# Optimization experiments

Hardware: AMD Instinct MI355X
Metric: run time of the kernel (lower is better)

Reference implementation:

```python
import jax, jax.numpy as jnp
import numpy as np

B, H, W, L, C = 4, 64, 64, 64, 64
NB, BS, F = 8, 8, 1          # num_blocks, block_size, hidden_size_factor
R, ALPHA = 8, 1.0            # lora_r, lora_alpha
M, T = 32, 8                 # modes, temporal_modes
SCALE = 1.0 / (BS * BS * F)  # param init scale from the module


def setup_inputs() -> dict:
    key = jax.random.key(0)
    ks = jax.random.split(key, 14)
    d = {"x": jax.random.normal(ks[0], (B, H, W, L, C), jnp.float32)}
    d["w1"] = SCALE * jax.random.uniform(ks[1], (2, NB, BS, BS * F), jnp.float32)
    d["b1"] = SCALE * jax.random.uniform(ks[2], (2, NB, BS * F), jnp.float32)
    d["w2"] = SCALE * jax.random.uniform(ks[3], (2, NB, BS * F, BS), jnp.float32)
    d["b2"] = SCALE * jax.random.uniform(ks[4], (2, NB, BS), jnp.float32)
    names = ["la1rA", "la1rB", "la1iA", "la1iB", "la2rA", "la2rB", "la2iA", "la2iB"]
    shapes = [(NB, BS, R), (NB, R, BS * F), (NB, BS, R), (NB, R, BS * F),
              (NB, BS * F, R), (NB, R, BS), (NB, BS * F, R), (NB, R, BS)]
    for i, (n, s) in enumerate(zip(names, shapes)):
        d[n] = 0.02 * jax.random.normal(ks[5 + i], s, jnp.float32)
    return d


def _afno(x, w1, b1, w2, b2, la1rA, la1rB, la1iA, la1iB, la2rA, la2rB, la2iA, la2iB):
    s = ALPHA / R
    # effective per-block weights: base + LoRA low-rank update  [NB, in, out]
    W1r = w1[0] + s * jnp.einsum('nir,nro->nio', la1rA, la1rB)
    W1i = w1[1] + s * jnp.einsum('nir,nro->nio', la1iA, la1iB)
    W2r = w2[0] + s * jnp.einsum('nir,nro->nio', la2rA, la2rB)
    W2i = w2[1] + s * jnp.einsum('nir,nro->nio', la2iA, la2iB)

    xf = jnp.fft.rfftn(x, axes=(1, 2, 3), norm='ortho')      # [B,H,W,L//2+1,C] complex
    Lh = xf.shape[3]
    xs = xf[:, :M, :M, :T].reshape(B, M, M, T, NB, BS)        # truncated modes, block split
    xr, xi = xs.real, xs.imag

    def lin(v, Wb, bb):  # block-diagonal linear: [...,n,i] x [n,i,o] + [n,o]
        return jnp.einsum('bxyzni,nio->bxyzno', v, Wb) + bb

    gelu = lambda t: jax.nn.gelu(t, approximate=False)
    o1r = gelu(lin(xr, W1r, b1[0]) - lin(xi, W1i, b1[1]))
    o1i = gelu(lin(xi, W1r, b1[0]) + lin(xr, W1i, b1[1]))
    o2r = lin(o1r, W2r, b2[0]) - lin(o1i, W2i, b2[1])
    o2i = lin(o1i, W2r, b2[0]) + lin(o1r, W2i, b2[1])

    o2 = (o2r + 1j * o2i).reshape(B, M, M, T, C)
    full = jnp.zeros((B, H, W, Lh, C), dtype=xf.dtype).at[:, :M, :M, :T].set(o2)
    out = jnp.fft.irfftn(full, s=(H, W, L), axes=(1, 2, 3), norm='ortho')
    return out + x


def reference(x, w1, b1, w2, b2, la1rA, la1rB, la1iA, la1iB, la2rA, la2rB, la2iA, la2iB):
    return _afno(x, w1, b1, w2, b2, la1rA, la1rB, la1iA, la1iB, la2rA, la2rB, la2iA, la2iB)
```

## Files before the change

### kernel.cpp

```cpp
#include <hip/hip_runtime.h>
#include <math.h>


#define PI2_64 0.09817477042468103f

__device__ __forceinline__ float gelu_exact(float t) {
    return 0.5f * t * (1.0f + erff(t * 0.7071067811865475f));
}

__device__ __forceinline__ unsigned int f2bf(float f) {
    unsigned int u = __float_as_uint(f);
    return (u + 0x7FFFu + ((u >> 16) & 1u)) >> 16;
}
__device__ __forceinline__ uint2 pack4(float4 f) {
    return make_uint2(f2bf(f.x) | (f2bf(f.y) << 16),
                      f2bf(f.z) | (f2bf(f.w) << 16));
}
__device__ __forceinline__ float4 unpack4(uint2 u) {
    return make_float4(__uint_as_float(u.x << 16),
                       __uint_as_float(u.x & 0xFFFF0000u),
                       __uint_as_float(u.y << 16),
                       __uint_as_float(u.y & 0xFFFF0000u));
}

__global__ void __launch_bounds__(256) k1a_dft_l(const float* __restrict__ x,
                                                 unsigned int* __restrict__ y1f) {
    __shared__ float2 twT[8][32];
    int tid = threadIdx.x;
    if (tid < 256) {
        int k = tid >> 5, l = tid & 31;
        float s, c;
        sincosf(PI2_64 * (float)((k * l) & 63), &s, &c);
        twT[k][l] = make_float2(c, s);
    }
    __syncthreads();

    int bid = blockIdx.x;
    int wg = bid & 3, bh = bid >> 2;
    int cq = tid & 15, wl = tid >> 4;
    int w = wg * 16 + wl;
    const float* xp = x + (size_t)(bh * 64 + w) * 4096 + 4 * cq;

    float4 A0[8], A1[8];
#pragma unroll
    for (int kl = 0; kl < 8; ++kl) {
        A0[kl] = make_float4(0.f, 0.f, 0.f, 0.f);
        A1[kl] = make_float4(0.f, 0.f, 0.f, 0.f);
    }

    for (int l0 = 0; l0 < 32; l0 += 2) {
        float4 v0  = *(const float4*)(xp + (l0 + 0) * 64);
        float4 v0p = *(const float4*)(xp + (l0 + 32) * 64);
        float4 v1  = *(const float4*)(xp + (l0 + 1) * 64);
        float4 v1p = *(const float4*)(xp + (l0 + 33) * 64);
        float4 E0 = make_float4(v0.x + v0p.x, v0.y + v0p.y, v0.z + v0p.z, v0.w + v0p.w);
        float4 O0 = make_float4(v0.x - v0p.x, v0.y - v0p.y, v0.z - v0p.z, v0.w - v0p.w);
        float4 E1 = make_float4(v1.x + v1p.x, v1.y + v1p.y, v1.z + v1p.z, v1.w + v1p.w);
        float4 O1 = make_float4(v1.x - v1p.x, v1.y - v1p.y, v1.z - v1p.z, v1.w - v1p.w);
#pragma unroll
        for (int kl = 0; kl < 8; ++kl) {
            float2 t0 = twT[kl][l0];
            float2 t1 = twT[kl][l0 + 1];
            float4 s0 = (kl & 1) ? O0 : E0;
            float4 s1 = (kl & 1) ? O1 : E1;
            A0[kl].x += s0.x * t0.x;  A0[kl].y -= s0.x * t0.y;
            A0[kl].z += s0.y * t0.x;  A0[kl].w -= s0.y * t0.y;
            A1[kl].x += s0.z * t0.x;  A1[kl].y -= s0.z * t0.y;
            A1[kl].z += s0.w * t0.x;  A1[kl].w -= s0.w * t0.y;
            A0[kl].x += s1.x * t1.x;  A0[kl].y -= s1.x * t1.y;
            A0[kl].z += s1.y * t1.x;  A0[kl].w -= s1.y * t1.y;
            A1[kl].x += s1.z * t1.x;  A1[kl].y -= s1.z * t1.y;
            A1[kl].z += s1.w * t1.x;  A1[kl].w -= s1.w * t1.y;
        }
    }
    uint4* y1 = (uint4*)y1f;
    size_t base = (size_t)bh * 8192 + (size_t)w * 16 + cq;
#pragma unroll
    for (int kl = 0; kl < 8; ++kl) {
        uint2 p0 = pack4(A0[kl]);
        uint2 p1 = pack4(A1[kl]);
        y1[base + kl * 1024] = make_uint4(p0.x, p0.y, p1.x, p1.y);
    }
}

__global__ void __launch_bounds__(256) k1b_dft_w(const unsigned int* __restrict__ y1f,
                                                 unsigned int* __restrict__ y2f) {
    __shared__ float4 sD[64 * 32];
    __shared__ float2 twT[32][32];
    int tid = threadIdx.x;
#pragma unroll
    for (int e = 0; e < 4; ++e) {
        int idx = e * 256 + tid;
        int k = idx >> 5, l = idx & 31;
        float s, c;
        sincosf(PI2_64 * (float)((k * l) & 63), &s, &c);
        twT[k][l] = make_float2(c, s);
    }
    int pos = blockIdx.x;
    int kl = pos & 7, bh = pos >> 3;
    const uint2* src = (const uint2*)y1f + (size_t)pos * 2048;
#pragma unroll
    for (int r = 0; r < 8; ++r)
        sD[r * 256 + tid] = unpack4(src[r * 256 + tid]);
    __syncthreads();

    int cp = tid & 31, kwg = tid >> 5;
    float4 acc[4];
#pragma unroll
    for (int i = 0; i < 4; ++i) acc[i] = make_float4(0.f, 0.f, 0.f, 0.f);

    for (int w = 0; w < 32; ++w) {
        float4 d  = sD[w * 32 + cp];
        float4 dp = sD[(w + 32) * 32 + cp];
        float4 E = make_float4(d.x + dp.x, d.y + dp.y, d.z + dp.z, d.w + dp.w);
        float4 O = make_float4(d.x - dp.x, d.y - dp.y, d.z - dp.z, d.w - dp.w);
#pragma unroll
        for (int i = 0; i < 4; ++i) {
            float2 t = twT[kwg * 4 + i][w];
            float4 s = (i & 1) ? O : E;
            acc[i].x += s.x * t.x + s.y * t.y;
            acc[i].y += s.y * t.x - s.x * t.y;
            acc[i].z += s.z * t.x + s.w * t.y;
            acc[i].w += s.w * t.x - s.z * t.y;
        }
    }
    int b = bh >> 6, h = bh & 63;
    uint2* y2 = (uint2*)y2f;
#pragma unroll
    for (int i = 0; i < 4; ++i) {
        int kw = kwg * 4 + i;
        y2[((size_t)((b * 8 + kl) * 32 + kw) * 64 + h) * 32 + cp] = pack4(acc[i]);
    }
}

__global__ void __launch_bounds__(256) kc_h_mlp(
        const unsigned int* __restrict__ y2f, unsigned int* __restrict__ z2f,
        const float* __restrict__ w1, const float* __restrict__ b1,
        const float* __restrict__ w2, const float* __restrict__ b2,
        const float* __restrict__ la1rA, const float* __restrict__ la1rB,
        const float* __restrict__ la1iA, const float* __restrict__ la1iB,
        const float* __restrict__ la2rA, const float* __restrict__ la2rB,
        const float* __restrict__ la2iA, const float* __restrict__ la2iB) {
    __shared__ float2 sD[64][64];
    __shared__ float2 sT[32][34];
    __shared__ float2 sM[32][66];
    __shared__ float  sW[4][512];
    __shared__ float  sb1[128], sb2[128];
    int tid = threadIdx.x;
    int pos = blockIdx.x;
    int kl = pos & 7, kw = (pos >> 3) & 31, b = pos >> 8;

#pragma unroll
    for (int r = 0; r < 4; ++r) {
        int idx = r * 256 + tid;
        int h = idx >> 5, kh = idx & 31;
        float sn, cs;
        sincosf(PI2_64 * (float)((h * kh) & 63), &sn, &cs);
        sT[h][kh] = make_float2(cs, -sn);
    }
    const uint2* src = (const uint2*)y2f + (size_t)((b * 8 + kl) * 32 + kw) * 2048;
#pragma unroll
    for (int r = 0; r < 8; ++r) {
        int idx = r * 256 + tid;
        *(float4*)(&sD[idx >> 5][(idx & 31) * 2]) = unpack4(src[idx]);
    }
    {
        const float* As[4]   = {la1rA, la1iA, la2rA, la2iA};
        const float* Bs[4]   = {la1rB, la1iB, la2rB, la2iB};
        const float* base[4] = {w1, w1 + 512, w2, w2 + 512};
#pragma unroll
        for (int e = 0; e < 8; ++e) {
            int flat = tid + e * 256;
            int mat = flat >> 9;
            int rem = flat & 511;
            int n = rem >> 6, i = (rem >> 3) & 7, o = rem & 7;
            const float* A  = As[mat] + n * 64 + i * 8;
            const float* Bp = Bs[mat] + n * 64 + o;
            float s = 0.f;
#pragma unroll
            for (int r = 0; r < 8; ++r) s += A[r] * Bp[r * 8];
            sW[mat][(i * 8 + o) * 8 + n] = base[mat][n * 64 + i * 8 + o] + 0.125f * s;
        }
        if (tid < 128) sb1[tid] = b1[tid];
        else           sb2[tid - 128] = b2[tid - 128];
    }
    __syncthreads();

    {
        float4* sd4 = (float4*)&sD[0][0];
#pragma unroll
        for (int r = 0; r < 4; ++r) {
            int idx = r * 256 + tid;
            int h = idx >> 5, cq = idx & 31;
            float4 a = sd4[h * 32 + cq];
            float4 c = sd4[(h + 32) * 32 + cq];
            sd4[h * 32 + cq]        = make_float4(a.x + c.x, a.y + c.y, a.z + c.z, a.w + c.w);
            sd4[(h + 32) * 32 + cq] = make_float4(a.x - c.x, a.y - c.y, a.z - c.z, a.w - c.w);
        }
    }
    __syncthreads();

    {
        int kh0 = (tid >> 5) * 4;
        int c0  = (tid & 31) * 2;
        float mr[4][2], mi[4][2];
#pragma unroll
        for (int i = 0; i < 4; ++i)
#pragma unroll
            for (int j = 0; j < 2; ++j) { mr[i][j] = 0.f; mi[i][j] = 0.f; }
        for (int h = 0; h < 32; ++h) {
            float4 dE = *(const float4*)(&sD[h][c0]);
            float4 dO = *(const float4*)(&sD[h + 32][c0]);
            float Er[2] = {dE.x, dE.z}, Ei[2] = {dE.y, dE.w};
            float Or[2] = {dO.x, dO.z}, Oi[2] = {dO.y, dO.w};
            const float4* tT = (const float4*)(&sT[h][kh0]);
            float4 u0 = tT[0], u1 = tT[1];
            float Tr[4] = {u0.x, u0.z, u1.x, u1.z};
            float Ti[4] = {u0.y, u0.w, u1.y, u1.w};
#pragma unroll
            for (int i = 0; i < 4; ++i) {
                const float* Dr = (i & 1) ? Or : Er;
                const float* Di = (i & 1) ? Oi : Ei;
#pragma unroll
                for (int j = 0; j < 2; ++j) {
                    mr[i][j] += Tr[i] * Dr[j] - Ti[i] * Di[j];
                    mi[i][j] += Tr[i] * Di[j] + Ti[i] * Dr[j];
                }
            }
        }
        const float sc = 1.0f / 512.0f;
#pragma unroll
        for (int i = 0; i < 4; ++i)
#pragma unroll
            for (int j = 0; j < 2; ++j)
                sM[kh0 + i][c0 + j] = make_float2(mr[i][j] * sc, mi[i][j] * sc);
    }
    __syncthreads();

    float2* sM2 = (float2*)&sD[0][0];
    {
        int kh = tid >> 3, n = tid & 7;
        float xr[8], xi[8];
#pragma unroll
        for (int i = 0; i < 8; ++i) {
            float2 v = sM[kh][n * 8 + i];
            xr[i] = v.x; xi[i] = v.y;
        }
        float o1r[8], o1i[8];
#pragma unroll
        for (int o = 0; o < 8; ++o) {
            float br = sb1[n * 8 + o], bi = sb1[64 + n * 8 + o];
            float sr = br - bi, si = br + bi;
#pragma unroll
            for (int i = 0; i < 8; ++i) {
                float wr = sW[0][(i * 8 + o) * 8 + n];
                float wi = sW[1][(i * 8 + o) * 8 + n];
                sr += xr[i] * wr - xi[i] * wi;
                si += xi[i] * wr + xr[i] * wi;
            }
            o1r[o] = gelu_exact(sr);
            o1i[o] = gelu_exact(si);
        }
#pragma unroll
        for (int o = 0; o < 8; ++o) {
            float br = sb2[n * 8 + o], bi = sb2[64 + n * 8 + o];
            float sr = br - bi, si = br + bi;
#pragma unroll
            for (int i = 0; i < 8; ++i) {
                float wr = sW[2][(i * 8 + o) * 8 + n];
                float wi = sW[3][(i * 8 + o) * 8 + n];
                sr += o1r[i] * wr - o1i[i] * wi;
                si += o1i[i] * wr + o1r[i] * wi;
            }
            sM2[kh * 66 + n * 8 + o] = make_float2(sr, si);
        }
    }
    __syncthreads();

    {
        int h0 = (tid >> 4) * 2;
        int c0 = (tid & 15) * 4;
        float SEr[2][4], SEi[2][4], SOr[2][4], SOi[2][4];
#pragma unroll
        for (int r = 0; r < 2; ++r)
#pragma unroll
            for (int j = 0; j < 4; ++j) {
                SEr[r][j] = 0.f; SEi[r][j] = 0.f;
                SOr[r][j] = 0.f; SOi[r][j] = 0.f;
            }
        for (int khp = 0; khp < 16; ++khp) {
#pragma unroll
            for (int par = 0; par < 2; ++par) {
                int kh = 2 * khp + par;
                float2 T0 = sT[h0 + 0][kh];
                float2 T1 = sT[h0 + 1][kh];
                const float4* tM = (const float4*)(sM2 + kh * 66 + c0);
                float4 m0 = tM[0], m1 = tM[1];
                float Mr[4] = {m0.x, m0.z, m1.x, m1.z};
                float Mi[4] = {m0.y, m0.w, m1.y, m1.w};
                float (*Sr)[4] = par ? SOr : SEr;
                float (*Si)[4] = par ? SOi : SEi;
                float Tr[2] = {T0.x, T1.x};
                float Ti[2] = {T0.y, T1.y};
#pragma unroll
                for (int r = 0; r < 2; ++r)
#pragma unroll
                    for (int j = 0; j < 4; ++j) {
                        Sr[r][j] += Tr[r] * Mr[j] + Ti[r] * Mi[j];
                        Si[r][j] += Tr[r] * Mi[j] - Ti[r] * Mr[j];
                    }
            }
        }
        uint2* dst = (uint2*)z2f + (size_t)((b * 8 + kl) * 32 + kw) * 2048;
#pragma unroll
        for (int r = 0; r < 2; ++r) {
            int iA = (h0 + r) * 32 + (c0 >> 1);
            dst[iA]     = pack4(make_float4(SEr[r][0] + SOr[r][0], SEi[r][0] + SOi[r][0],
                                            SEr[r][1] + SOr[r][1], SEi[r][1] + SOi[r][1]));
            dst[iA + 1] = pack4(make_float4(SEr[r][2] + SOr[r][2], SEi[r][2] + SOi[r][2],
                                            SEr[r][3] + SOr[r][3], SEi[r][3] + SOi[r][3]));
            int iB = (h0 + 32 + r) * 32 + (c0 >> 1);
            dst[iB]     = pack4(make_float4(SEr[r][0] - SOr[r][0], SEi[r][0] - SOi[r][0],
                                            SEr[r][1] - SOr[r][1], SEi[r][1] - SOi[r][1]));
            dst[iB + 1] = pack4(make_float4(SEr[r][2] - SOr[r][2], SEi[r][2] - SOi[r][2],
                                            SEr[r][3] - SOr[r][3], SEi[r][3] - SOi[r][3]));
        }
    }
}

__global__ void __launch_bounds__(256) k3a_idft_w(const unsigned int* __restrict__ z2f,
                                                  unsigned int* __restrict__ zwf) {
    __shared__ float4 sZ[2 * 32 * 32];
    __shared__ float2 twT[32][32];
    int tid = threadIdx.x;
#pragma unroll
    for (int e = 0; e < 4; ++e) {
        int idx = e * 256 + tid;
        int w = idx >> 5, kw = idx & 31;
        float s, c;
        sincosf(PI2_64 * (float)((w * kw) & 63), &s, &c);
        twT[w][kw] = make_float2(c, s);
    }
    int bid = blockIdx.x;
    int klq = bid & 3, h = (bid >> 2) & 63, b = bid >> 8;
    const uint2* z2 = (const uint2*)z2f;
#pragma unroll
    for (int r = 0; r < 8; ++r) {
        int idx = r * 256 + tid;
        int row = idx >> 5, cp2 = idx & 31;
        int kli = row >> 5, kw = row & 31;
        sZ[idx] = unpack4(
            z2[((size_t)((b * 8 + klq * 2 + kli) * 32 + kw) * 64 + h) * 32 + cp2]);
    }
    __syncthreads();

    int cp = tid & 31, wq = tid >> 5;

    float4 E[2][4], O[2][4];
#pragma unroll
    for (int kli = 0; kli < 2; ++kli)
#pragma unroll
        for (int j = 0; j < 4; ++j) {
            E[kli][j] = make_float4(0.f, 0.f, 0.f, 0.f);
            O[kli][j] = make_float4(0.f, 0.f, 0.f, 0.f);
        }

    for (int kw = 0; kw < 32; kw += 2) {
#pragma unroll
        for (int kli = 0; kli < 2; ++kli) {
            float4 d = sZ[(kli * 32 + kw) * 32 + cp];
#pragma unroll
            for (int j = 0; j < 4; ++j) {
                float2 t = twT[wq * 4 + j][kw];
                E[kli][j].x += d.x * t.x - d.y * t.y;
                E[kli][j].y += d.y * t.x + d.x * t.y;
                E[kli][j].z += d.z * t.x - d.w * t.y;
                E[kli][j].w += d.w * t.x + d.z * t.y;
            }
        }
#pragma unroll
        for (int kli = 0; kli < 2; ++kli) {
            float4 d = sZ[(kli * 32 + kw + 1) * 32 + cp];
#pragma unroll
            for (int j = 0; j < 4; ++j) {
                float2 t = twT[wq * 4 + j][kw + 1];
                O[kli][j].x += d.x * t.x - d.y * t.y;
                O[kli][j].y += d.y * t.x + d.x * t.y;
                O[kli][j].z += d.z * t.x - d.w * t.y;
                O[kli][j].w += d.w * t.x + d.z * t.y;
            }
        }
    }
    uint2* zw = (uint2*)zwf;
    size_t slab = ((size_t)(b * 64 + h)) * 16384;
#pragma unroll
    for (int kli = 0; kli < 2; ++kli) {
        int kl = klq * 2 + kli;
#pragma unroll
        for (int j = 0; j < 4; ++j) {
            int w = wq * 4 + j;
            float4 e = E[kli][j], o = O[kli][j];
            zw[slab + ((size_t)w * 8 + kl) * 32 + cp] =
                pack4(make_float4(e.x + o.x, e.y + o.y, e.z + o.z, e.w + o.w));
            zw[slab + ((size_t)(w + 32) * 8 + kl) * 32 + cp] =
                pack4(make_float4(e.x - o.x, e.y - o.y, e.z - o.z, e.w - o.w));
        }
    }
}

__global__ void __launch_bounds__(256) k3b_idft_l(const float* __restrict__ x,
                                                  const unsigned int* __restrict__ zwf,
                                                  float* __restrict__ outp) {
    __shared__ float2 twA[8][32];
    int tid = threadIdx.x;
    if (tid < 256) {
        int k = tid >> 5, l = tid & 31;
        float s, c;
        sincosf(PI2_64 * (float)((k * l) & 63), &s, &c);
        twA[k][l] = make_float2(c, s);
    }
    __syncthreads();

    int bid = blockIdx.x;
    int wg = bid & 3, bh = bid >> 2;
    int cq = tid & 15, wl = tid >> 4;
    int w = wg * 16 + wl;

    const uint4* zw4 = (const uint4*)zwf;
    size_t zbase = ((size_t)(bh * 64 + w)) * 128 + cq;
    float4 z0[8], z1[8];
#pragma unroll
    for (int kl = 0; kl < 8; ++kl) {
        uint4 u = zw4[zbase + kl * 16];
        z0[kl] = unpack4(make_uint2(u.x, u.y));
        z1[kl] = unpack4(make_uint2(u.z, u.w));
    }

    float r00 = z0[0].x, r01 = z0[0].z;
    float r10 = z1[0].x, r11 = z1[0].z;
#pragma unroll
    for (int kl = 1; kl < 8; ++kl) {
        z0[kl].x *= 2.f; z0[kl].y *= 2.f; z0[kl].z *= 2.f; z0[kl].w *= 2.f;
        z1[kl].x *= 2.f; z1[kl].y *= 2.f; z1[kl].z *= 2.f; z1[kl].w *= 2.f;
    }
    const size_t row = ((size_t)(bh * 64 + w)) * 4096;
    const float* xp = x + row + 4 * cq;
    float* op = outp + row + 4 * cq;
    const float sc = 1.0f / 512.0f;

    for (int l = 0; l < 32; ++l) {
        float4 a0 = *(const float4*)(xp + l * 64);
        float4 a1 = *(const float4*)(xp + (l + 32) * 64);
        float e00 = 0.f, e01 = 0.f, e10 = 0.f, e11 = 0.f;
        float o00 = 0.f, o01 = 0.f, o10 = 0.f, o11 = 0.f;
#pragma unroll
        for (int kl = 2; kl < 8; kl += 2) {
            float2 t = twA[kl][l];
            e00 += z0[kl].x * t.x - z0[kl].y * t.y;
            e01 += z0[kl].z * t.x - z0[kl].w * t.y;
            e10 += z1[kl].x * t.x - z1[kl].y * t.y;
            e11 += z1[kl].z * t.x - z1[kl].w * t.y;
        }
#pragma unroll
        for (int kl = 1; kl < 8; kl += 2) {
            float2 t = twA[kl][l];
            o00 += z0[kl].x * t.x - z0[kl].y * t.y;
            o01 += z0[kl].z * t.x - z0[kl].w * t.y;
            o10 += z1[kl].x * t.x - z1[kl].y * t.y;
            o11 += z1[kl].z * t.x - z1[kl].w * t.y;
        }
        float b00 = r00 + e00, b01 = r01 + e01;
        float b10 = r10 + e10, b11 = r11 + e11;
        *(float4*)(op + l * 64) = make_float4(
            (b00 + o00) * sc + a0.x, (b01 + o01) * sc + a0.y,
            (b10 + o10) * sc + a0.z, (b11 + o11) * sc + a0.w);
        *(float4*)(op + (l + 32) * 64) = make_float4(
            (b00 - o00) * sc + a1.x, (b01 - o01) * sc + a1.y,
            (b10 - o10) * sc + a1.z, (b11 - o11) * sc + a1.w);
    }
}

extern "C" void kernel_launch(void* const* d_in, const int* in_sizes, int n_in,
                              void* d_out, int out_size, void* d_ws, size_t ws_size,
                              hipStream_t stream) {
    const float* x     = (const float*)d_in[0];
    const float* w1    = (const float*)d_in[1];
    const float* b1    = (const float*)d_in[2];
    const float* w2    = (const float*)d_in[3];
    const float* b2    = (const float*)d_in[4];
    const float* la1rA = (const float*)d_in[5];
    const float* la1rB = (const float*)d_in[6];
    const float* la1iA = (const float*)d_in[7];
    const float* la1iB = (const float*)d_in[8];
    const float* la2rA = (const float*)d_in[9];
    const float* la2rB = (const float*)d_in[10];
    const float* la2iA = (const float*)d_in[11];
    const float* la2iB = (const float*)d_in[12];
    float* out = (float*)d_out;

    unsigned int* ws = (unsigned int*)d_ws;
    unsigned int* y1 = ws;
    unsigned int* y2 = ws + 8388608;
    unsigned int* z2 = ws + 12582912;
    unsigned int* zw = ws + 16777216;

    hipLaunchKernelGGL(k1a_dft_l,  dim3(1024), dim3(256), 0, stream, x, y1);
    hipLaunchKernelGGL(k1b_dft_w,  dim3(2048), dim3(256), 0, stream, y1, y2);
    hipLaunchKernelGGL(kc_h_mlp,   dim3(1024), dim3(256), 0, stream, y2, z2,
                       w1, b1, w2, b2, la1rA, la1rB, la1iA, la1iB,
                       la2rA, la2rB, la2iA, la2iB);
    hipLaunchKernelGGL(k3a_idft_w, dim3(1024), dim3(256), 0, stream, z2, zw);
    hipLaunchKernelGGL(k3b_idft_l, dim3(1024), dim3(256), 0, stream, x, zw, out);
}
```

Before: 306.1 us.

## Fuse L and W forward DFT kernels via shared memory, keep mlp buffers bf16

```diff
diff --git a/kernel.cpp b/kernel.cpp
--- a/kernel.cpp
+++ b/kernel.cpp
@@ -22,114 +22,106 @@
                        __uint_as_float(u.y << 16),
                        __uint_as_float(u.y & 0xFFFF0000u));
 }
-
-__global__ void __launch_bounds__(256) k1a_dft_l(const float* __restrict__ x,
-                                                 unsigned int* __restrict__ y1f) {
-    __shared__ float2 twT[8][32];
+__device__ __forceinline__ unsigned int pack2(float r, float i) {
+    return f2bf(r) | (f2bf(i) << 16);
+}
+__device__ __forceinline__ float2 unpack2(unsigned int u) {
+    return make_float2(__uint_as_float(u << 16),
+                       __uint_as_float(u & 0xFFFF0000u));
+}
+
+__global__ void __launch_bounds__(256) k1_fused(const float* __restrict__ x,
+                                                unsigned int* __restrict__ y2f) {
+    __shared__ uint2  sY[8 * 1089];
+    __shared__ float2 twT1[8][32];
+    __shared__ float2 twT2[32][32];
     int tid = threadIdx.x;
-    if (tid < 256) {
+    {
         int k = tid >> 5, l = tid & 31;
         float s, c;
         sincosf(PI2_64 * (float)((k * l) & 63), &s, &c);
-        twT[k][l] = make_float2(c, s);
-    }
-    __syncthreads();
-
-    int bid = blockIdx.x;
-    int wg = bid & 3, bh = bid >> 2;
-    int cq = tid & 15, wl = tid >> 4;
-    int w = wg * 16 + wl;
-    const float* xp = x + (size_t)(bh * 64 + w) * 4096 + 4 * cq;
-
-    float4 A0[8], A1[8];
-#pragma unroll
-    for (int kl = 0; kl < 8; ++kl) {
-        A0[kl] = make_float4(0.f, 0.f, 0.f, 0.f);
-        A1[kl] = make_float4(0.f, 0.f, 0.f, 0.f);
-    }
-
-    for (int l0 = 0; l0 < 32; l0 += 2) {
-        float4 v0  = *(const float4*)(xp + (l0 + 0) * 64);
-        float4 v0p = *(const float4*)(xp + (l0 + 32) * 64);
-        float4 v1  = *(const float4*)(xp + (l0 + 1) * 64);
-        float4 v1p = *(const float4*)(xp + (l0 + 33) * 64);
-        float4 E0 = make_float4(v0.x + v0p.x, v0.y + v0p.y, v0.z + v0p.z, v0.w + v0p.w);
-        float4 O0 = make_float4(v0.x - v0p.x, v0.y - v0p.y, v0.z - v0p.z, v0.w - v0p.w);
-        float4 E1 = make_float4(v1.x + v1p.x, v1.y + v1p.y, v1.z + v1p.z, v1.w + v1p.w);
-        float4 O1 = make_float4(v1.x - v1p.x, v1.y - v1p.y, v1.z - v1p.z, v1.w - v1p.w);
-#pragma unroll
-        for (int kl = 0; kl < 8; ++kl) {
-            float2 t0 = twT[kl][l0];
-            float2 t1 = twT[kl][l0 + 1];
-            float4 s0 = (kl & 1) ? O0 : E0;
-            float4 s1 = (kl & 1) ? O1 : E1;
-            A0[kl].x += s0.x * t0.x;  A0[kl].y -= s0.x * t0.y;
-            A0[kl].z += s0.y * t0.x;  A0[kl].w -= s0.y * t0.y;
-            A1[kl].x += s0.z * t0.x;  A1[kl].y -= s0.z * t0.y;
-            A1[kl].z += s0.w * t0.x;  A1[kl].w -= s0.w * t0.y;
-            A0[kl].x += s1.x * t1.x;  A0[kl].y -= s1.x * t1.y;
-            A0[kl].z += s1.y * t1.x;  A0[kl].w -= s1.y * t1.y;
-            A1[kl].x += s1.z * t1.x;  A1[kl].y -= s1.z * t1.y;
-            A1[kl].z += s1.w * t1.x;  A1[kl].w -= s1.w * t1.y;
-        }
-    }
-    uint4* y1 = (uint4*)y1f;
-    size_t base = (size_t)bh * 8192 + (size_t)w * 16 + cq;
-#pragma unroll
-    for (int kl = 0; kl < 8; ++kl) {
-        uint2 p0 = pack4(A0[kl]);
-        uint2 p1 = pack4(A1[kl]);
-        y1[base + kl * 1024] = make_uint4(p0.x, p0.y, p1.x, p1.y);
-    }
-}
-
-__global__ void __launch_bounds__(256) k1b_dft_w(const unsigned int* __restrict__ y1f,
-                                                 unsigned int* __restrict__ y2f) {
-    __shared__ float4 sD[64 * 32];
-    __shared__ float2 twT[32][32];
-    int tid = threadIdx.x;
+        twT1[k][l] = make_float2(c, s);
+    }
 #pragma unroll
     for (int e = 0; e < 4; ++e) {
         int idx = e * 256 + tid;
         int k = idx >> 5, l = idx & 31;
         float s, c;
         sincosf(PI2_64 * (float)((k * l) & 63), &s, &c);
-        twT[k][l] = make_float2(c, s);
-    }
-    int pos = blockIdx.x;
-    int kl = pos & 7, bh = pos >> 3;
-    const uint2* src = (const uint2*)y1f + (size_t)pos * 2048;
-#pragma unroll
-    for (int r = 0; r < 8; ++r)
-        sD[r * 256 + tid] = unpack4(src[r * 256 + tid]);
-    __syncthreads();
-
-    int cp = tid & 31, kwg = tid >> 5;
-    float4 acc[4];
-#pragma unroll
-    for (int i = 0; i < 4; ++i) acc[i] = make_float4(0.f, 0.f, 0.f, 0.f);
-
-    for (int w = 0; w < 32; ++w) {
-        float4 d  = sD[w * 32 + cp];
-        float4 dp = sD[(w + 32) * 32 + cp];
-        float4 E = make_float4(d.x + dp.x, d.y + dp.y, d.z + dp.z, d.w + dp.w);
-        float4 O = make_float4(d.x - dp.x, d.y - dp.y, d.z - dp.z, d.w - dp.w);
-#pragma unroll
-        for (int i = 0; i < 4; ++i) {
-            float2 t = twT[kwg * 4 + i][w];
-            float4 s = (i & 1) ? O : E;
-            acc[i].x += s.x * t.x + s.y * t.y;
-            acc[i].y += s.y * t.x - s.x * t.y;
-            acc[i].z += s.z * t.x + s.w * t.y;
-            acc[i].w += s.w * t.x - s.z * t.y;
-        }
-    }
-    int b = bh >> 6, h = bh & 63;
-    uint2* y2 = (uint2*)y2f;
-#pragma unroll
-    for (int i = 0; i < 4; ++i) {
-        int kw = kwg * 4 + i;
-        y2[((size_t)((b * 8 + kl) * 32 + kw) * 64 + h) * 32 + cp] = pack4(acc[i]);
+        twT2[k][l] = make_float2(c, s);
+    }
+    __syncthreads();
+
+    int bid = blockIdx.x;
+    int ch = bid & 1, bh = bid >> 1;
+
+    {
+        int cp = tid & 15, wl = tid >> 4;
+#pragma unroll
+        for (int wi = 0; wi < 4; ++wi) {
+            int w = wi * 16 + wl;
+            const float* xp = x + (size_t)(bh * 64 + w) * 4096 + ch * 32 + 2 * cp;
+            float4 A[8];
+#pragma unroll
+            for (int kl = 0; kl < 8; ++kl) A[kl] = make_float4(0.f, 0.f, 0.f, 0.f);
+            for (int l0 = 0; l0 < 32; l0 += 2) {
+                float2 v0  = *(const float2*)(xp + (l0 + 0) * 64);
+                float2 v0p = *(const float2*)(xp + (l0 + 32) * 64);
+                float2 v1  = *(const float2*)(xp + (l0 + 1) * 64);
+                float2 v1p = *(const float2*)(xp + (l0 + 33) * 64);
+                float2 E0 = make_float2(v0.x + v0p.x, v0.y + v0p.y);
+                float2 O0 = make_float2(v0.x - v0p.x, v0.y - v0p.y);
+                float2 E1 = make_float2(v1.x + v1p.x, v1.y + v1p.y);
+                float2 O1 = make_float2(v1.x - v1p.x, v1.y - v1p.y);
+#pragma unroll
+                for (int kl = 0; kl < 8; ++kl) {
+                    float2 t0 = twT1[kl][l0];
+                    float2 t1 = twT1[kl][l0 + 1];
+                    float2 s0 = (kl & 1) ? O0 : E0;
+                    float2 s1 = (kl & 1) ? O1 : E1;
+                    A[kl].x += s0.x * t0.x;  A[kl].y -= s0.x * t0.y;
+                    A[kl].z += s0.y * t0.x;  A[kl].w -= s0.y * t0.y;
+                    A[kl].x += s1.x * t1.x;  A[kl].y -= s1.x * t1.y;
+                    A[kl].z += s1.y * t1.x;  A[kl].w -= s1.y * t1.y;
+                }
+            }
+#pragma unroll
+            for (int kl = 0; kl < 8; ++kl)
+                sY[kl * 1089 + w * 17 + cp] = pack4(A[kl]);
+        }
+    }
+    __syncthreads();
+
+    {
+        int cp = tid & 15, kl = (tid >> 4) & 7, kwh = tid >> 7;
+        const uint2* row = &sY[kl * 1089];
+        float4 acc[16];
+#pragma unroll
+        for (int i = 0; i < 16; ++i) acc[i] = make_float4(0.f, 0.f, 0.f, 0.f);
+
+        for (int w = 0; w < 32; ++w) {
+            float4 a = unpack4(row[w * 17 + cp]);
+            float4 b4 = unpack4(row[(w + 32) * 17 + cp]);
+            float4 E = make_float4(a.x + b4.x, a.y + b4.y, a.z + b4.z, a.w + b4.w);
+            float4 O = make_float4(a.x - b4.x, a.y - b4.y, a.z - b4.z, a.w - b4.w);
+#pragma unroll
+            for (int i = 0; i < 16; ++i) {
+                float2 t = twT2[kwh * 16 + i][w];
+                float4 s = (i & 1) ? O : E;
+                acc[i].x += s.x * t.x + s.y * t.y;
+                acc[i].y += s.y * t.x - s.x * t.y;
+                acc[i].z += s.z * t.x + s.w * t.y;
+                acc[i].w += s.w * t.x - s.z * t.y;
+            }
+        }
+        int b = bh >> 6, h = bh & 63;
+        uint2* y2 = (uint2*)y2f;
+#pragma unroll
+        for (int i = 0; i < 16; ++i) {
+            int kw = kwh * 16 + i;
+            y2[((size_t)((b * 8 + kl) * 32 + kw) * 64 + h) * 32 + ch * 16 + cp] =
+                pack4(acc[i]);
+        }
     }
 }
 
@@ -141,11 +133,12 @@
         const float* __restrict__ la1iA, const float* __restrict__ la1iB,
         const float* __restrict__ la2rA, const float* __restrict__ la2rB,
         const float* __restrict__ la2iA, const float* __restrict__ la2iB) {
-    __shared__ float2 sD[64][64];
+    __shared__ uint2  sDu[64 * 32];
     __shared__ float2 sT[32][34];
-    __shared__ float2 sM[32][66];
+    __shared__ unsigned int sMu[32 * 66];
     __shared__ float  sW[4][512];
     __shared__ float  sb1[128], sb2[128];
+    unsigned int* sM2u = (unsigned int*)sDu;
     int tid = threadIdx.x;
     int pos = blockIdx.x;
     int kl = pos & 7, kw = (pos >> 3) & 31, b = pos >> 8;
@@ -162,7 +155,7 @@
 #pragma unroll
     for (int r = 0; r < 8; ++r) {
         int idx = r * 256 + tid;
-        *(float4*)(&sD[idx >> 5][(idx & 31) * 2]) = unpack4(src[idx]);
+        sDu[idx] = src[idx];
     }
     {
         const float* As[4]   = {la1rA, la1iA, la2rA, la2iA};
@@ -187,32 +180,21 @@
     __syncthreads();
 
     {
-        float4* sd4 = (float4*)&sD[0][0];
-#pragma unroll
-        for (int r = 0; r < 4; ++r) {
-            int idx = r * 256 + tid;
-            int h = idx >> 5, cq = idx & 31;
-            float4 a = sd4[h * 32 + cq];
-            float4 c = sd4[(h + 32) * 32 + cq];
-            sd4[h * 32 + cq]        = make_float4(a.x + c.x, a.y + c.y, a.z + c.z, a.w + c.w);
-            sd4[(h + 32) * 32 + cq] = make_float4(a.x - c.x, a.y - c.y, a.z - c.z, a.w - c.w);
-        }
-    }
-    __syncthreads();
-
-    {
         int kh0 = (tid >> 5) * 4;
-        int c0  = (tid & 31) * 2;
+        int cq  = tid & 31;
+        int c0f = cq * 2;
         float mr[4][2], mi[4][2];
 #pragma unroll
         for (int i = 0; i < 4; ++i)
 #pragma unroll
             for (int j = 0; j < 2; ++j) { mr[i][j] = 0.f; mi[i][j] = 0.f; }
         for (int h = 0; h < 32; ++h) {
-            float4 dE = *(const float4*)(&sD[h][c0]);
-            float4 dO = *(const float4*)(&sD[h + 32][c0]);
-            float Er[2] = {dE.x, dE.z}, Ei[2] = {dE.y, dE.w};
-            float Or[2] = {dO.x, dO.z}, Oi[2] = {dO.y, dO.w};
+            float4 a  = unpack4(sDu[h * 32 + cq]);
+            float4 c4 = unpack4(sDu[(h + 32) * 32 + cq]);
+            float Er[2] = {a.x + c4.x, a.z + c4.z};
+            float Ei[2] = {a.y + c4.y, a.w + c4.w};
+            float Or[2] = {a.x - c4.x, a.z - c4.z};
+            float Oi[2] = {a.y - c4.y, a.w - c4.w};
             const float4* tT = (const float4*)(&sT[h][kh0]);
             float4 u0 = tT[0], u1 = tT[1];
             float Tr[4] = {u0.x, u0.z, u1.x, u1.z};
@@ -233,17 +215,16 @@
         for (int i = 0; i < 4; ++i)
 #pragma unroll
             for (int j = 0; j < 2; ++j)
-                sM[kh0 + i][c0 + j] = make_float2(mr[i][j] * sc, mi[i][j] * sc);
-    }
-    __syncthreads();
-
-    float2* sM2 = (float2*)&sD[0][0];
+                sMu[(kh0 + i) * 66 + c0f + j] = pack2(mr[i][j] * sc, mi[i][j] * sc);
+    }
+    __syncthreads();
+
     {
         int kh = tid >> 3, n = tid & 7;
         float xr[8], xi[8];
 #pragma unroll
         for (int i = 0; i < 8; ++i) {
-            float2 v = sM[kh][n * 8 + i];
+            float2 v = unpack2(sMu[kh * 66 + n * 8 + i]);
             xr[i] = v.x; xi[i] = v.y;
         }
         float o1r[8], o1i[8];
@@ -272,7 +253,7 @@
                 sr += o1r[i] * wr - o1i[i] * wi;
                 si += o1i[i] * wr + o1r[i] * wi;
             }
-            sM2[kh * 66 + n * 8 + o] = make_float2(sr, si);
+            sM2u[kh * 66 + n * 8 + o] = pack2(sr, si);
         }
     }
     __syncthreads();
@@ -294,10 +275,13 @@
                 int kh = 2 * khp + par;
                 float2 T0 = sT[h0 + 0][kh];
                 float2 T1 = sT[h0 + 1][kh];
-                const float4* tM = (const float4*)(sM2 + kh * 66 + c0);
-                float4 m0 = tM[0], m1 = tM[1];
-                float Mr[4] = {m0.x, m0.z, m1.x, m1.z};
-                float Mi[4] = {m0.y, m0.w, m1.y, m1.w};
+                const unsigned int* mp = sM2u + kh * 66 + c0;
+                uint2 ua = *(const uint2*)(mp);
+                uint2 ub = *(const uint2*)(mp + 2);
+                float2 m0 = unpack2(ua.x), m1 = unpack2(ua.y);
+                float2 m2 = unpack2(ub.x), m3 = unpack2(ub.y);
+                float Mr[4] = {m0.x, m1.x, m2.x, m3.x};
+                float Mi[4] = {m0.y, m1.y, m2.y, m3.y};
                 float (*Sr)[4] = par ? SOr : SEr;
                 float (*Si)[4] = par ? SOi : SEi;
                 float Tr[2] = {T0.x, T1.x};
@@ -499,13 +483,11 @@
     float* out = (float*)d_out;
 
     unsigned int* ws = (unsigned int*)d_ws;
-    unsigned int* y1 = ws;
-    unsigned int* y2 = ws + 8388608;
-    unsigned int* z2 = ws + 12582912;
-    unsigned int* zw = ws + 16777216;
-
-    hipLaunchKernelGGL(k1a_dft_l,  dim3(1024), dim3(256), 0, stream, x, y1);
-    hipLaunchKernelGGL(k1b_dft_w,  dim3(2048), dim3(256), 0, stream, y1, y2);
+    unsigned int* y2 = ws;
+    unsigned int* z2 = ws + 4194304;
+    unsigned int* zw = ws + 8388608;
+
+    hipLaunchKernelGGL(k1_fused,   dim3(512),  dim3(256), 0, stream, x, y2);
     hipLaunchKernelGGL(kc_h_mlp,   dim3(1024), dim3(256), 0, stream, y2, z2,
                        w1, b1, w2, b2, la1rA, la1rB, la1iA, la1iB,
                        la2rA, la2rB, la2iA, la2iB);
```

After: 282.2 us, median of 2. -7.8%, faster.
